# Performance work log

Measured on AMD Instinct MI355X. Metric: run time of the kernel, lower is better.

The kernel has to match this reference:

```python
import jax, jax.numpy as jnp
import numpy as np

VOCAB = 100000
DIM = 300
BATCH = 8192
WINDOW = 5
NEG = 5


def _init_table(key):
    # row 0 is padding (zeros); rest uniform(-0.5/D, 0.5/D) per the torch init
    tail = jax.random.uniform(key, (VOCAB - 1, DIM), dtype=jnp.float32,
                              minval=-0.5 / DIM, maxval=0.5 / DIM)
    return jnp.concatenate([jnp.zeros((1, DIM), jnp.float32), tail], axis=0)


def setup_inputs() -> dict:
    key = jax.random.key(0)
    k1, k2, k3, k4, k5 = jax.random.split(key, 5)
    return {
        "i_emb": _init_table(k1),                                              # [V, D]
        "o_emb": _init_table(k2),                                              # [V, D]
        "i_word": jax.random.randint(k3, (BATCH,), 0, VOCAB),                  # [B]
        "o_word": jax.random.randint(k4, (BATCH, 2 * WINDOW), 0, VOCAB),       # [B, 2W]
        "n_word": jax.random.randint(k5, (BATCH, 2 * WINDOW * NEG), 0, VOCAB), # [B, 2W*NEG]
    }


def reference(i_emb, o_emb, i_word, o_word, n_word):
    i_vec = i_emb[i_word]            # [B, D]
    o_vec = o_emb[o_word]            # [B, 2W, D]
    n_vec = -o_emb[n_word]           # [B, 2W*NEG, D] (negated, per .neg())

    # log(sigmoid(x)) computed stably as log_sigmoid
    o_score = jnp.einsum('bcd,bd->bc', o_vec, i_vec)   # [B, 2W]
    n_score = jnp.einsum('bnd,bd->bn', n_vec, i_vec)   # [B, 2W*NEG]

    oloss = jax.nn.log_sigmoid(o_score).mean(axis=1)   # [B]
    nloss = jax.nn.log_sigmoid(n_score).reshape(-1, 2 * WINDOW, NEG).sum(axis=2).mean(axis=1)  # [B]
    return -(oloss + nloss).mean()
```

## Files before the change

### kernel.cpp

```cpp
#include <hip/hip_runtime.h>

#define VOCAB 100000
#define DIM   300
#define BATCH 8192
#define NPOS  10
#define NNEG  50
#define NTOT  60

__device__ __forceinline__ float log_sigmoid(float x) {
    return fminf(x, 0.0f) - log1pf(__expf(-fabsf(x)));
}

template <int PATTERN>
__device__ __forceinline__ float swz_xor(float p) {
    return __int_as_float(__builtin_amdgcn_ds_swizzle(__float_as_int(p), PATTERN));
}

__global__ __launch_bounds__(256) void sgns_partial(
    const float* __restrict__ i_emb, const float* __restrict__ o_emb,
    const int* __restrict__ i_word, const int* __restrict__ o_word,
    const int* __restrict__ n_word, float* __restrict__ partial)
{
    __shared__ float4 ivec[75];
    __shared__ int   sidx[NTOT];
    __shared__ float gsum[16];

    const int b = blockIdx.x;
    const int t = threadIdx.x;
    const int g = t >> 4;
    const int q = t & 15;

    const float4* irow = (const float4*)(i_emb + (long)i_word[b] * DIM);
    if (t < 75) ivec[t] = irow[t];
    if (t < NPOS)       sidx[t] = o_word[b * NPOS + t];
    else if (t < NTOT)  sidx[t] = n_word[b * NNEG + (t - NPOS)];
    __syncthreads();

    const float4 iv0 = ivec[q];
    const float4 iv1 = ivec[q + 16];
    const float4 iv2 = ivec[q + 32];
    const float4 iv3 = ivec[q + 48];
    const float4 iv4 = (q < 11) ? ivec[q + 64] : make_float4(0.f, 0.f, 0.f, 0.f);

    float acc = 0.f;
    #pragma unroll
    for (int k = 0; k < 4; ++k) {
        const int j = g + 16 * k;
        if (j < NTOT) {
            const float4* row = (const float4*)(o_emb + (long)sidx[j] * DIM);
            float4 r0 = row[q];
            float4 r1 = row[q + 16];
            float4 r2 = row[q + 32];
            float4 r3 = row[q + 48];
            float p = r0.x * iv0.x + r0.y * iv0.y + r0.z * iv0.z + r0.w * iv0.w;
            p += r1.x * iv1.x + r1.y * iv1.y + r1.z * iv1.z + r1.w * iv1.w;
            p += r2.x * iv2.x + r2.y * iv2.y + r2.z * iv2.z + r2.w * iv2.w;
            p += r3.x * iv3.x + r3.y * iv3.y + r3.z * iv3.z + r3.w * iv3.w;
            if (q < 11) {
                float4 r4 = row[q + 64];
                p += r4.x * iv4.x + r4.y * iv4.y + r4.z * iv4.z + r4.w * iv4.w;
            }
            p += swz_xor<0x041F>(p);
            p += swz_xor<0x081F>(p);
            p += swz_xor<0x101F>(p);
            p += swz_xor<0x201F>(p);
            acc += log_sigmoid(j < NPOS ? p : -p);
        }
    }

    if (q == 0) gsum[g] = acc;
    __syncthreads();
    if (t == 0) {
        float s = 0.f;
        #pragma unroll
        for (int i = 0; i < 16; ++i) s += gsum[i];
        partial[b] = s;
    }
}

__global__ __launch_bounds__(256) void sgns_finalize(
    const float* __restrict__ partial, float* __restrict__ out)
{
    const int t = threadIdx.x;
    const float4* p4 = (const float4*)partial;
    float s = 0.f;
    #pragma unroll
    for (int i = 0; i < BATCH / 4 / 256; ++i) {
        float4 v = p4[t + 256 * i];
        s += v.x + v.y + v.z + v.w;
    }
    #pragma unroll
    for (int o = 32; o > 0; o >>= 1) s += __shfl_xor(s, o, 64);
    __shared__ float ws[4];
    if ((t & 63) == 0) ws[t >> 6] = s;
    __syncthreads();
    if (t == 0) out[0] = -(ws[0] + ws[1] + ws[2] + ws[3]) / (float)(BATCH * NPOS);
}

extern "C" void kernel_launch(void* const* d_in, const int* in_sizes, int n_in,
                              void* d_out, int out_size, void* d_ws, size_t ws_size,
                              hipStream_t stream) {
    const float* i_emb  = (const float*)d_in[0];
    const float* o_emb  = (const float*)d_in[1];
    const int*   i_word = (const int*)d_in[2];
    const int*   o_word = (const int*)d_in[3];
    const int*   n_word = (const int*)d_in[4];
    float* partial = (float*)d_ws;
    float* out     = (float*)d_out;

    sgns_partial<<<BATCH, 256, 0, stream>>>(i_emb, o_emb, i_word, o_word, n_word, partial);
    sgns_finalize<<<1, 256, 0, stream>>>(partial, out);
}
```

Baseline: 286.8 us.

## Convert output embedding table to padded bf16 before gathering rows

Each call first converts the whole o_emb table into a bf16 copy in the workspace, with each row padded to 640 bytes. The gather kernel then reads these half-size rows and computes dot products in fp32 against the fp32 input vector. This cuts the bytes moved by the random row gather, in exchange for a full-table conversion pass and reduced precision. If the workspace is too small, the original fp32 path runs instead; launch bounds and the loop guard were also adjusted.

```diff
diff --git a/kernel.cpp b/kernel.cpp
--- a/kernel.cpp
+++ b/kernel.cpp
@@ -7,6 +7,9 @@
 #define NNEG  50
 #define NTOT  60
 
+#define ROWB  640
+#define OBF_BYTES (100000ull * ROWB)
+
 __device__ __forceinline__ float log_sigmoid(float x) {
     return fminf(x, 0.0f) - log1pf(__expf(-fabsf(x)));
 }
@@ -16,7 +19,100 @@
     return __int_as_float(__builtin_amdgcn_ds_swizzle(__float_as_int(p), PATTERN));
 }
 
-__global__ __launch_bounds__(256) void sgns_partial(
+__device__ __forceinline__ unsigned bf16rne(float f) {
+    unsigned u = __float_as_uint(f);
+    return (u + 0x7fffu + ((u >> 16) & 1u)) >> 16;
+}
+
+__device__ __forceinline__ float dot8(uint4 u, float4 va, float4 vb) {
+    float s;
+    s  = __uint_as_float(u.x << 16) * va.x + __uint_as_float(u.x & 0xffff0000u) * va.y;
+    s += __uint_as_float(u.y << 16) * va.z + __uint_as_float(u.y & 0xffff0000u) * va.w;
+    s += __uint_as_float(u.z << 16) * vb.x + __uint_as_float(u.z & 0xffff0000u) * vb.y;
+    s += __uint_as_float(u.w << 16) * vb.z + __uint_as_float(u.w & 0xffff0000u) * vb.w;
+    return s;
+}
+
+__global__ __launch_bounds__(128) void conv_bf16(
+    const float* __restrict__ o_emb, unsigned char* __restrict__ obf)
+{
+    const int row = blockIdx.x;
+    const int t   = threadIdx.x;
+    if (t >= 80) return;
+    uint2 outv = make_uint2(0u, 0u);
+    if (t < 75) {
+        float4 v = ((const float4*)(o_emb + (size_t)row * DIM))[t];
+        outv.x = bf16rne(v.x) | (bf16rne(v.y) << 16);
+        outv.y = bf16rne(v.z) | (bf16rne(v.w) << 16);
+    }
+    ((uint2*)(obf + (size_t)row * ROWB))[t] = outv;
+}
+
+__global__ __launch_bounds__(256, 4) void sgns_partial_bf16(
+    const float* __restrict__ i_emb, const unsigned char* __restrict__ obf,
+    const int* __restrict__ i_word, const int* __restrict__ o_word,
+    const int* __restrict__ n_word, float* __restrict__ partial)
+{
+    __shared__ float4 ivec[80];
+    __shared__ int   sidx[NTOT];
+    __shared__ float gsum[16];
+
+    const int b = blockIdx.x;
+    const int t = threadIdx.x;
+    const int g = t >> 4;
+    const int q = t & 15;
+
+    const float4* irow = (const float4*)(i_emb + (long)i_word[b] * DIM);
+    if (t < 75) ivec[t] = irow[t];
+    else if (t < 80) ivec[t] = make_float4(0.f, 0.f, 0.f, 0.f);
+    if (t < NPOS)       sidx[t] = o_word[b * NPOS + t];
+    else if (t < NTOT)  sidx[t] = n_word[b * NNEG + (t - NPOS)];
+    __syncthreads();
+
+    const int nwords = (g < 12) ? 4 : 3;
+
+    uint4 r[4][3];
+    #pragma unroll
+    for (int k = 0; k < 4; ++k) {
+        if (k < nwords) {
+            const uint4* row = (const uint4*)(obf + (size_t)sidx[g + 16 * k] * ROWB);
+            r[k][0] = row[q];
+            r[k][1] = row[q + 16];
+            if (q < 6) r[k][2] = row[q + 32];
+        }
+    }
+
+    const float4 a0 = ivec[2 * q],      a1 = ivec[2 * q + 1];
+    const float4 b0 = ivec[2 * q + 32], b1 = ivec[2 * q + 33];
+    float4 c0, c1;
+    if (q < 6) { c0 = ivec[2 * q + 64]; c1 = ivec[2 * q + 65]; }
+
+    float acc = 0.f;
+    #pragma unroll
+    for (int k = 0; k < 4; ++k) {
+        if (k < nwords) {
+            const int j = g + 16 * k;
+            float p = dot8(r[k][0], a0, a1) + dot8(r[k][1], b0, b1);
+            if (q < 6) p += dot8(r[k][2], c0, c1);
+            p += swz_xor<0x041F>(p);
+            p += swz_xor<0x081F>(p);
+            p += swz_xor<0x101F>(p);
+            p += swz_xor<0x201F>(p);
+            acc += log_sigmoid(j < NPOS ? p : -p);
+        }
+    }
+
+    if (q == 0) gsum[g] = acc;
+    __syncthreads();
+    if (t == 0) {
+        float s = 0.f;
+        #pragma unroll
+        for (int i = 0; i < 16; ++i) s += gsum[i];
+        partial[b] = s;
+    }
+}
+
+__global__ __launch_bounds__(256, 4) void sgns_partial_f32(
     const float* __restrict__ i_emb, const float* __restrict__ o_emb,
     const int* __restrict__ i_word, const int* __restrict__ o_word,
     const int* __restrict__ n_word, float* __restrict__ partial)
@@ -42,11 +138,12 @@
     const float4 iv3 = ivec[q + 48];
     const float4 iv4 = (q < 11) ? ivec[q + 64] : make_float4(0.f, 0.f, 0.f, 0.f);
 
+    const int nwords = (g < 12) ? 4 : 3;
     float acc = 0.f;
     #pragma unroll
     for (int k = 0; k < 4; ++k) {
-        const int j = g + 16 * k;
-        if (j < NTOT) {
+        if (k < nwords) {
+            const int j = g + 16 * k;
             const float4* row = (const float4*)(o_emb + (long)sidx[j] * DIM);
             float4 r0 = row[q];
             float4 r1 = row[q + 16];
@@ -105,9 +202,18 @@
     const int*   i_word = (const int*)d_in[2];
     const int*   o_word = (const int*)d_in[3];
     const int*   n_word = (const int*)d_in[4];
-    float* partial = (float*)d_ws;
-    float* out     = (float*)d_out;
-
-    sgns_partial<<<BATCH, 256, 0, stream>>>(i_emb, o_emb, i_word, o_word, n_word, partial);
-    sgns_finalize<<<1, 256, 0, stream>>>(partial, out);
-}
+    float* out = (float*)d_out;
+
+    const size_t need = OBF_BYTES + (size_t)BATCH * 4;
+    if (ws_size >= need) {
+        unsigned char* obf = (unsigned char*)d_ws;
+        float* partial = (float*)(obf + OBF_BYTES);
+        conv_bf16<<<VOCAB, 128, 0, stream>>>(o_emb, obf);
+        sgns_partial_bf16<<<BATCH, 256, 0, stream>>>(i_emb, obf, i_word, o_word, n_word, partial);
+        sgns_finalize<<<1, 256, 0, stream>>>(partial, out);
+    } else {
+        float* partial = (float*)d_ws;
+        sgns_partial_f32<<<BATCH, 256, 0, stream>>>(i_emb, o_emb, i_word, o_word, n_word, partial);
+        sgns_finalize<<<1, 256, 0, stream>>>(partial, out);
+    }
+}
```

New measurement: 275.7 us. 1.04x faster.
